# Performance work log

Hardware: AMD Instinct MI355X
Metric: run time of the kernel (lower is better)

Reference implementation:

```python
import jax, jax.numpy as jnp
import numpy as np

H = 8        # n_heads (== n_kv_heads)
D = 128      # head_dim
WINDOW = 16  # sliding window (left); causal => right window = 0
EPS = 1e-6   # qk_norm_eps


def rms_norm(x, w, eps=EPS):
    # RMSNorm over last dim with learnable scale
    ms = jnp.mean(jnp.square(x), axis=-1, keepdims=True)
    return x * jax.lax.rsqrt(ms + eps) * w


def setup_inputs() -> dict:
    key = jax.random.key(0)
    ks = jax.random.split(key, 5)
    B, S, dim = 4, 2048, 1024
    scale = 1.0 / np.sqrt(dim)
    return {
        "x": jax.random.normal(ks[0], (B, S, dim), jnp.float32),
        "wq": jax.random.normal(ks[1], (dim, dim), jnp.float32) * scale,
        "wk": jax.random.normal(ks[2], (dim, dim), jnp.float32) * scale,
        "wv": jax.random.normal(ks[3], (dim, dim), jnp.float32) * scale,
        "wo": jax.random.normal(ks[4], (dim, dim), jnp.float32) * scale,
        "q_norm_w": jnp.ones((dim,), jnp.float32),
        "k_norm_w": jnp.ones((dim,), jnp.float32),
    }


def reference(x, wq, wk, wv, wo, q_norm_w, k_norm_w):
    B, S, dim = x.shape
    # projections (torch Linear: x @ W.T)
    xq = rms_norm(x @ wq.T, q_norm_w)
    xk = rms_norm(x @ wk.T, k_norm_w)
    xv = x @ wv.T
    q = xq.reshape(B, S, H, D)
    k = xk.reshape(B, S, H, D)
    v = xv.reshape(B, S, H, D)

    # ALiBi slopes for 8 heads (power of two): 2^-1 .. 2^-8
    slopes = jnp.exp2(-jnp.arange(1, H + 1, dtype=jnp.float32))
    pos = jnp.arange(S)
    rel = pos[None, :] - pos[:, None]          # [S, S], rel[i, j] = j - i
    bias = slopes[:, None, None] * rel.astype(x.dtype)   # [H, S, S]
    masked = (rel > 0) | (rel < -WINDOW)       # causal + sliding window
    bias = jnp.where(masked[None], -jnp.inf, bias)

    scores = jnp.einsum('bqhd,bkhd->bhqk', q, k) / np.sqrt(D) + bias[None]
    attn = jax.nn.softmax(scores, axis=-1)
    out = jnp.einsum('bhqk,bkhd->bqhd', attn, v).reshape(B, S, H * D)
    return out @ wo.T
```

## Files before the change

kernel.cpp:

```cpp
#include <hip/hip_runtime.h>
#include <math.h>

#define NHEADS 8
#define HDIM   128
#define WIN    16
#define DIM    1024
#define QKVDIM 3072
#define SEQ    2048
#define BATCH  4
#define MROWS  (BATCH * SEQ)
#define RMS_EPS 1e-6f
#define PLANE  ((size_t)MROWS * HDIM)

typedef __bf16 bf16x8 __attribute__((ext_vector_type(8)));
typedef unsigned short u16x8 __attribute__((ext_vector_type(8)));
typedef float  f32x4  __attribute__((ext_vector_type(4)));

__device__ __forceinline__ unsigned short f2b(float f) {
    union { float f; unsigned u; } c; c.f = f;
    return (unsigned short)((c.u + 0x7FFFu + ((c.u >> 16) & 1u)) >> 16);
}
__device__ __forceinline__ float b2f(unsigned short u) {
    union { unsigned u; float f; } c; c.u = ((unsigned)u) << 16; return c.f;
}
__device__ __forceinline__ bf16x8 u2b(u16x8 u) {
    union { u16x8 u; bf16x8 b; } c; c.u = u; return c.b;
}

__global__ __launch_bounds__(256) void cast_all(const float* __restrict__ x,
                                                const float* __restrict__ w0,
                                                const float* __restrict__ w1,
                                                const float* __restrict__ w2,
                                                const float* __restrict__ w3,
                                                unsigned short* __restrict__ xb,
                                                unsigned short* __restrict__ wb,
                                                float* __restrict__ sumsq)
{
    const int b = blockIdx.x;
    const int t = threadIdx.x;
    if (b >= 12288) {
        ((float4*)sumsq)[(b - 12288) * 256 + t] = make_float4(0.f, 0.f, 0.f, 0.f);
        return;
    }
    const float* src;
    unsigned short* dst;
    int i;
    if (b < 8192) {
        i = b * 256 + t;
        src = x; dst = xb;
    } else {
        const int bb = b - 8192;
        const int which = bb >> 10;
        i = (bb & 1023) * 256 + t;
        src = which == 0 ? w0 : which == 1 ? w1 : which == 2 ? w2 : w3;
        dst = wb + (size_t)which * DIM * DIM;
    }
    const float4 v = ((const float4*)src)[i];
    ushort4 o;
    o.x = f2b(v.x); o.y = f2b(v.y); o.z = f2b(v.z); o.w = f2b(v.w);
    ((ushort4*)dst)[i] = o;
}

#define BARR do { asm volatile("s_barrier" ::: "memory"); __builtin_amdgcn_sched_barrier(0); } while (0)
#define WAITV(N) asm volatile("s_waitcnt vmcnt(" #N ")" ::: "memory")

#define LDA8(b) { \
    _Pragma("unroll") for (int il = 0; il < 4; ++il) { \
        const int rr = (wm * 64 + il * 16 + frow) * 64; \
        af[il][0] = *(const bf16x8*)&As[b][rr + cs0]; \
        af[il][1] = *(const bf16x8*)&As[b][rr + cs1]; \
    } }

#define LDB4(bh, b, bgr) { \
    _Pragma("unroll") for (int jl = 0; jl < 2; ++jl) { \
        const int rr = (wn * 64 + (bh) * 32 + jl * 16 + frow) * 64; \
        bgr[jl][0] = *(const bf16x8*)&Bs[b][rr + cs0]; \
        bgr[jl][1] = *(const bf16x8*)&Bs[b][rr + cs1]; \
    } }

#define MMA16(bh, bgr) { \
    __builtin_amdgcn_s_setprio(1); \
    _Pragma("unroll") for (int il = 0; il < 4; ++il) \
    _Pragma("unroll") for (int jl = 0; jl < 2; ++jl) { \
        acc[il][(bh)*2+jl] = __builtin_amdgcn_mfma_f32_16x16x32_bf16(af[il][0], bgr[jl][0], acc[il][(bh)*2+jl], 0, 0, 0); \
        acc[il][(bh)*2+jl] = __builtin_amdgcn_mfma_f32_16x16x32_bf16(af[il][1], bgr[jl][1], acc[il][(bh)*2+jl], 0, 0, 0); \
    } \
    __builtin_amdgcn_s_setprio(0); }

#define STAGE_A(b, kt) { \
    _Pragma("unroll") for (int s2 = 0; s2 < 4; ++s2) { \
        const int rb = s2 * 32; \
        __builtin_amdgcn_global_load_lds( \
            (const __attribute__((address_space(1))) void*)(gA + (size_t)rb * K + (kt)), \
            (__attribute__((address_space(3))) void*)&As[b][(rb + wid * 8) * 64], 16, 0, 0); \
    } }

#define STAGE_B(b, kt) { \
    _Pragma("unroll") for (int s2 = 0; s2 < 4; ++s2) { \
        const int rb = s2 * 32; \
        __builtin_amdgcn_global_load_lds( \
            (const __attribute__((address_space(1))) void*)(gB + (size_t)rb * K + (kt)), \
            (__attribute__((address_space(3))) void*)&Bs[b][(rb + wid * 8) * 64], 16, 0, 0); \
    } }

template <typename TC, bool PLANAR>
__global__ __launch_bounds__(256, 2) void gemm_nt_128(const unsigned short* __restrict__ A,
                                                      const unsigned short* __restrict__ B,
                                                      TC* __restrict__ C,
                                                      float* __restrict__ sumsq,
                                                      int M, int N, int K)
{
    __shared__ __align__(16) __bf16 As[2][128 * 64];
    __shared__ __align__(16) __bf16 Bs[2][128 * 64];

    const int t    = threadIdx.x;
    const int wid  = t >> 6;
    const int lane = t & 63;
    const int wm   = wid >> 1;
    const int wn   = wid & 1;
    const int bm0  = blockIdx.y * 128;
    const int bn0  = blockIdx.x * 128;

    const int frow = lane & 15;
    const int quad = lane >> 4;
    const int cs0  = ((quad    ) ^ (frow & 7)) * 8;
    const int cs1  = ((quad + 4) ^ (frow & 7)) * 8;

    const int lr = lane >> 3;
    const int lc = (lane & 7) ^ lr;
    const unsigned short* gA = A + (size_t)(bm0 + wid * 8 + lr) * K + lc * 8;
    const unsigned short* gB = B + (size_t)(bn0 + wid * 8 + lr) * K + lc * 8;

    f32x4 acc[4][4];
    #pragma unroll
    for (int i = 0; i < 4; ++i)
        #pragma unroll
        for (int j = 0; j < 4; ++j)
            #pragma unroll
            for (int e = 0; e < 4; ++e) acc[i][j][e] = 0.f;

    bf16x8 af[4][2], bg0[2][2], bg1[2][2];

    const int NI = K >> 6;

    STAGE_B(0, 0); STAGE_A(0, 0); STAGE_B(1, 64);
    WAITV(4);
    BARR;

    for (int i = 0; i < NI; ++i) {
        const int cur = i & 1;
        const int nxt = cur ^ 1;
        const int kt  = i << 6;
        LDA8(cur); LDB4(0, cur, bg0); LDB4(1, cur, bg1);
        if (i + 1 < NI) STAGE_A(nxt, kt + 64);
        BARR; MMA16(0, bg0); BARR;
        if (i + 2 < NI) STAGE_B(cur, kt + 128);
        BARR; MMA16(1, bg1);
        if (i + 2 < NI)      { WAITV(4); }
        else if (i + 1 < NI) { WAITV(0); }
        BARR;
    }

    const int m_base = bm0 + wm * 64;
    const int n_base = bn0 + wn * 64;
    if constexpr (PLANAR) {
        size_t cb[4];
        #pragma unroll
        for (int j = 0; j < 4; ++j) {
            const int nb = n_base + j * 16;
            cb[j] = (size_t)(nb >> 7) * PLANE + (nb & 127);
        }
        #pragma unroll
        for (int il = 0; il < 4; ++il)
            #pragma unroll
            for (int r = 0; r < 4; ++r) {
                const size_t row = m_base + il * 16 + quad * 4 + r;
                #pragma unroll
                for (int j = 0; j < 4; ++j)
                    ((unsigned short*)C)[cb[j] + row * HDIM + frow] = f2b(acc[il][j][r]);
            }
        if (sumsq != nullptr && bn0 < 2 * DIM) {
            const int which = bn0 >> 10;
            #pragma unroll
            for (int il = 0; il < 4; ++il)
                #pragma unroll
                for (int r = 0; r < 4; ++r) {
                    float p = acc[il][0][r] * acc[il][0][r] + acc[il][1][r] * acc[il][1][r]
                            + acc[il][2][r] * acc[il][2][r] + acc[il][3][r] * acc[il][3][r];
                    p += __shfl_xor(p, 1, 64);
                    p += __shfl_xor(p, 2, 64);
                    p += __shfl_xor(p, 4, 64);
                    p += __shfl_xor(p, 8, 64);
                    if (frow == 0)
                        atomicAdd(&sumsq[(size_t)(m_base + il * 16 + quad * 4 + r) * 2 + which], p);
                }
        }
    } else {
        #pragma unroll
        for (int il = 0; il < 4; ++il)
            #pragma unroll
            for (int r = 0; r < 4; ++r) {
                TC* crow = C + (size_t)(m_base + il * 16 + quad * 4 + r) * N + n_base + frow;
                #pragma unroll
                for (int j = 0; j < 4; ++j)
                    crow[j * 16] = acc[il][j][r];
            }
    }
}

__global__ __launch_bounds__(256) void attn_mfma(const unsigned short* __restrict__ qkvp,
                                                 const float* __restrict__ sumsq,
                                                 const float* __restrict__ qw,
                                                 const float* __restrict__ kw,
                                                 unsigned short* __restrict__ o)
{
    __shared__ __align__(16) unsigned short Klds[80 * 136];
    __shared__ __align__(16) unsigned short Vt[128 * 88];
    __shared__ __align__(16) unsigned short Plds[4 * 16 * 40];

    const int t  = threadIdx.x;
    const int qb = blockIdx.x;
    const int h  = blockIdx.y;
    const int r0 = qb * 64;
    const int i0 = r0 & (SEQ - 1);
    const int bb = r0 - i0;

    const unsigned short* qg = qkvp + (size_t)h * PLANE;
    const unsigned short* kg = qkvp + (size_t)(NHEADS + h) * PLANE;
    const unsigned short* vg = qkvp + (size_t)(2 * NHEADS + h) * PLANE;

    const int w    = t >> 6;
    const int lane = t & 63;
    const int frow = lane & 15;
    const int quad = lane >> 4;
    const int fk   = quad * 8;

    const size_t qrow = (size_t)(r0 + w * 16 + frow) * HDIM;
    u16x8 qa[4];
    #pragma unroll
    for (int kt = 0; kt < 4; ++kt)
        qa[kt] = *(const u16x8*)(qg + qrow + kt * 32 + fk);

    #pragma unroll
    for (int it = 0; it < 5; ++it) {
        const int c = it * 256 + t;
        {
            const int lr2 = c >> 4, c8 = c & 15;
            const int ks = i0 - 16 + lr2;
            const int rc = ks < 0 ? 0 : ks;
            const u16x8 kv = *(const u16x8*)(kg + (size_t)(bb + rc) * HDIM + c8 * 8);
            u16x8 ko;
            #pragma unroll
            for (int e = 0; e < 8; ++e) {
                const int d = h * HDIM + c8 * 8 + e;
                ko[e] = f2b(b2f(kv[e]) * qw[d] * kw[d]);
            }
            *(u16x8*)&Klds[lr2 * 136 + c8 * 8] = ko;
        }
        {
            const int c8 = c / 80, lr2 = c - c8 * 80;
            const int ks = i0 - 16 + lr2;
            const int rc = ks < 0 ? 0 : ks;
            const u16x8 vv = *(const u16x8*)(vg + (size_t)(bb + rc) * HDIM + c8 * 8);
            #pragma unroll
            for (int e = 0; e < 8; ++e)
                Vt[(c8 * 8 + e) * 88 + lr2] = vv[e];
        }
    }
    __syncthreads();

    const int kidx0 = i0 - 16 + w * 16 + frow;
    const int kr0   = kidx0 < 0 ? 0 : kidx0;

    f32x4 s0 = {0.f, 0.f, 0.f, 0.f}, s1 = {0.f, 0.f, 0.f, 0.f};
    #pragma unroll
    for (int kt = 0; kt < 4; ++kt) {
        const bf16x8 af = u2b(qa[kt]);
        const bf16x8 b0 = *(const bf16x8*)&Klds[(w * 16 + frow) * 136 + kt * 32 + fk];
        const bf16x8 b1 = *(const bf16x8*)&Klds[(w * 16 + 16 + frow) * 136 + kt * 32 + fk];
        s0 = __builtin_amdgcn_mfma_f32_16x16x32_bf16(af, b0, s0, 0, 0, 0);
        s1 = __builtin_amdgcn_mfma_f32_16x16x32_bf16(af, b1, s1, 0, 0, 0);
    }

    const float ksc0 = rsqrtf(sumsq[(size_t)(bb + kr0) * 2 + 1] * (1.0f / DIM) + RMS_EPS);
    const float ksc1 = rsqrtf(sumsq[(size_t)(r0 + w * 16 + frow) * 2 + 1] * (1.0f / DIM) + RMS_EPS);
    float qs[4];
    #pragma unroll
    for (int r = 0; r < 4; ++r)
        qs[r] = rsqrtf(sumsq[(size_t)(r0 + w * 16 + quad * 4 + r) * 2] * (1.0f / DIM) + RMS_EPS);

    const float scl   = 0.088388347648318447f;
    const float slope = exp2f(-(float)(h + 1));
    const bool  lead  = (i0 == 0) && (w == 0);
    const int   col   = frow;
    float inv[4];
    #pragma unroll
    for (int r = 0; r < 4; ++r) {
        const int m = quad * 4 + r;
        const float sc0 = scl * qs[r] * ksc0;
        const float sc1 = scl * qs[r] * ksc1;
        float v0 = (col < m || lead) ? -1e30f : s0[r] * sc0 + slope * (float)(col - 16 - m);
        float v1 = (col > m)         ? -1e30f : s1[r] * sc1 + slope * (float)(col - m);
        float mx = fmaxf(v0, v1);
        #pragma unroll
        for (int off = 1; off < 16; off <<= 1) mx = fmaxf(mx, __shfl_xor(mx, off, 64));
        const float e0 = __expf(v0 - mx);
        const float e1 = __expf(v1 - mx);
        float sm = e0 + e1;
        #pragma unroll
        for (int off = 1; off < 16; off <<= 1) sm += __shfl_xor(sm, off, 64);
        inv[r] = 1.0f / sm;
        Plds[(w * 16 + m) * 40 + col]      = f2b(e0);
        Plds[(w * 16 + m) * 40 + 16 + col] = f2b(e1);
    }

    const bf16x8 pf = *(const bf16x8*)&Plds[(w * 16 + frow) * 40 + fk];
    f32x4 oa[8];
    #pragma unroll
    for (int nt = 0; nt < 8; ++nt) {
        oa[nt][0] = 0.f; oa[nt][1] = 0.f; oa[nt][2] = 0.f; oa[nt][3] = 0.f;
        const bf16x8 vf = *(const bf16x8*)&Vt[(nt * 16 + frow) * 88 + w * 16 + fk];
        oa[nt] = __builtin_amdgcn_mfma_f32_16x16x32_bf16(pf, vf, oa[nt], 0, 0, 0);
    }

    #pragma unroll
    for (int nt = 0; nt < 8; ++nt)
        #pragma unroll
        for (int r = 0; r < 4; ++r) {
            const int m = quad * 4 + r;
            o[(size_t)(r0 + w * 16 + m) * DIM + h * HDIM + nt * 16 + col] =
                f2b(oa[nt][r] * inv[r]);
        }
}

extern "C" void kernel_launch(void* const* d_in, const int* in_sizes, int n_in,
                              void* d_out, int out_size, void* d_ws, size_t ws_size,
                              hipStream_t stream)
{
    const float* x  = (const float*)d_in[0];
    const float* wq = (const float*)d_in[1];
    const float* wk = (const float*)d_in[2];
    const float* wv = (const float*)d_in[3];
    const float* wo = (const float*)d_in[4];
    const float* qw = (const float*)d_in[5];
    const float* kw = (const float*)d_in[6];
    float* out = (float*)d_out;

    unsigned short* xb   = (unsigned short*)d_ws;
    unsigned short* wb   = xb + (size_t)MROWS * DIM;
    unsigned short* qkvp = wb + (size_t)4 * DIM * DIM;
    unsigned short* ob   = qkvp + (size_t)MROWS * QKVDIM;
    float*          ssq  = (float*)(ob + (size_t)MROWS * DIM);
    unsigned short* wob  = wb + (size_t)3 * DIM * DIM;

    cast_all<<<12304, 256, 0, stream>>>(x, wq, wk, wv, wo, xb, wb, ssq);

    gemm_nt_128<unsigned short, true><<<dim3(QKVDIM / 128, MROWS / 128), 256, 0, stream>>>(
        xb, wb, qkvp, ssq, MROWS, QKVDIM, DIM);

    attn_mfma<<<dim3(MROWS / 64, NHEADS), 256, 0, stream>>>(qkvp, ssq, qw, kw, ob);

    gemm_nt_128<float, false><<<dim3(DIM / 128, MROWS / 128), 256, 0, stream>>>(
        ob, wob, out, nullptr, MROWS, DIM, DIM);
}
```

Baseline: 203.2 us.

## Replace double-buffered GEMM pipeline with single-buffer loop and higher occupancy

Result: slower. 435.7 us (+114.4%).

```diff
diff --git a/kernel.cpp b/kernel.cpp
--- a/kernel.cpp
+++ b/kernel.cpp
@@ -61,57 +61,52 @@
     ((ushort4*)dst)[i] = o;
 }
 
-#define BARR do { asm volatile("s_barrier" ::: "memory"); __builtin_amdgcn_sched_barrier(0); } while (0)
-#define WAITV(N) asm volatile("s_waitcnt vmcnt(" #N ")" ::: "memory")
-
-#define LDA8(b) { \
+#define LDA8() { \
     _Pragma("unroll") for (int il = 0; il < 4; ++il) { \
         const int rr = (wm * 64 + il * 16 + frow) * 64; \
-        af[il][0] = *(const bf16x8*)&As[b][rr + cs0]; \
-        af[il][1] = *(const bf16x8*)&As[b][rr + cs1]; \
-    } }
-
-#define LDB4(bh, b, bgr) { \
+        af[il][0] = *(const bf16x8*)&As[rr + cs0]; \
+        af[il][1] = *(const bf16x8*)&As[rr + cs1]; \
+    } }
+
+#define LDB4(bh, bgr) { \
     _Pragma("unroll") for (int jl = 0; jl < 2; ++jl) { \
         const int rr = (wn * 64 + (bh) * 32 + jl * 16 + frow) * 64; \
-        bgr[jl][0] = *(const bf16x8*)&Bs[b][rr + cs0]; \
-        bgr[jl][1] = *(const bf16x8*)&Bs[b][rr + cs1]; \
+        bgr[jl][0] = *(const bf16x8*)&Bs[rr + cs0]; \
+        bgr[jl][1] = *(const bf16x8*)&Bs[rr + cs1]; \
     } }
 
 #define MMA16(bh, bgr) { \
-    __builtin_amdgcn_s_setprio(1); \
     _Pragma("unroll") for (int il = 0; il < 4; ++il) \
     _Pragma("unroll") for (int jl = 0; jl < 2; ++jl) { \
         acc[il][(bh)*2+jl] = __builtin_amdgcn_mfma_f32_16x16x32_bf16(af[il][0], bgr[jl][0], acc[il][(bh)*2+jl], 0, 0, 0); \
         acc[il][(bh)*2+jl] = __builtin_amdgcn_mfma_f32_16x16x32_bf16(af[il][1], bgr[jl][1], acc[il][(bh)*2+jl], 0, 0, 0); \
-    } \
-    __builtin_amdgcn_s_setprio(0); }
-
-#define STAGE_A(b, kt) { \
+    } }
+
+#define STAGE_A(kt) { \
     _Pragma("unroll") for (int s2 = 0; s2 < 4; ++s2) { \
         const int rb = s2 * 32; \
         __builtin_amdgcn_global_load_lds( \
             (const __attribute__((address_space(1))) void*)(gA + (size_t)rb * K + (kt)), \
-            (__attribute__((address_space(3))) void*)&As[b][(rb + wid * 8) * 64], 16, 0, 0); \
-    } }
-
-#define STAGE_B(b, kt) { \
+            (__attribute__((address_space(3))) void*)&As[(rb + wid * 8) * 64], 16, 0, 0); \
+    } }
+
+#define STAGE_B(kt) { \
     _Pragma("unroll") for (int s2 = 0; s2 < 4; ++s2) { \
         const int rb = s2 * 32; \
         __builtin_amdgcn_global_load_lds( \
             (const __attribute__((address_space(1))) void*)(gB + (size_t)rb * K + (kt)), \
-            (__attribute__((address_space(3))) void*)&Bs[b][(rb + wid * 8) * 64], 16, 0, 0); \
+            (__attribute__((address_space(3))) void*)&Bs[(rb + wid * 8) * 64], 16, 0, 0); \
     } }
 
 template <typename TC, bool PLANAR>
-__global__ __launch_bounds__(256, 2) void gemm_nt_128(const unsigned short* __restrict__ A,
+__global__ __launch_bounds__(256, 5) void gemm_nt_128(const unsigned short* __restrict__ A,
                                                       const unsigned short* __restrict__ B,
                                                       TC* __restrict__ C,
                                                       float* __restrict__ sumsq,
                                                       int M, int N, int K)
 {
-    __shared__ __align__(16) __bf16 As[2][128 * 64];
-    __shared__ __align__(16) __bf16 Bs[2][128 * 64];
+    __shared__ __align__(16) __bf16 As[128 * 64];
+    __shared__ __align__(16) __bf16 Bs[128 * 64];
 
     const int t    = threadIdx.x;
     const int wid  = t >> 6;
@@ -141,24 +136,12 @@
 
     bf16x8 af[4][2], bg0[2][2], bg1[2][2];
 
-    const int NI = K >> 6;
-
-    STAGE_B(0, 0); STAGE_A(0, 0); STAGE_B(1, 64);
-    WAITV(4);
-    BARR;
-
-    for (int i = 0; i < NI; ++i) {
-        const int cur = i & 1;
-        const int nxt = cur ^ 1;
-        const int kt  = i << 6;
-        LDA8(cur); LDB4(0, cur, bg0); LDB4(1, cur, bg1);
-        if (i + 1 < NI) STAGE_A(nxt, kt + 64);
-        BARR; MMA16(0, bg0); BARR;
-        if (i + 2 < NI) STAGE_B(cur, kt + 128);
-        BARR; MMA16(1, bg1);
-        if (i + 2 < NI)      { WAITV(4); }
-        else if (i + 1 < NI) { WAITV(0); }
-        BARR;
+    for (int kt = 0; kt < K; kt += 64) {
+        __syncthreads();
+        STAGE_A(kt); STAGE_B(kt);
+        __syncthreads();
+        LDA8(); LDB4(0, bg0); LDB4(1, bg1);
+        MMA16(0, bg0); MMA16(1, bg1);
     }
 
     const int m_base = bm0 + wm * 64;
```
